# Kernel tuning notes

Measured on AMD Instinct MI355X. Metric: run time of the kernel, lower is better.

Reference implementation:

```python
import jax, jax.numpy as jnp
import numpy as np

HIDDEN = 1024
N_HEADS = 16
HEAD_DIM = HIDDEN // N_HEADS  # 64; RoPE applied only to first HEAD_DIM channels (head 0)
NUM_BUCKETS = 32
MAX_DISTANCE = 128
MLP_HIDDEN = 4 * HIDDEN
B, N = 2, 2048


def _rotate_half(x):
    # interleaved pairs [a0,b0,a1,b1,...] -> [-b0,a0,-b1,a1,...]
    sh = x.shape
    xr = x.reshape(sh[:-1] + (sh[-1] // 2, 2))
    x1, x2 = xr[..., 0], xr[..., 1]
    return jnp.stack([-x2, x1], axis=-1).reshape(sh)


def _rel_bucket(n, num_buckets=NUM_BUCKETS, max_distance=MAX_DISTANCE):
    # bidirectional T5 bucketing
    ctx = jnp.arange(n)[:, None]
    mem = jnp.arange(n)[None, :]
    rp = mem - ctx  # [n, n]
    nb = num_buckets // 2
    buckets = jnp.where(rp > 0, nb, 0)
    rp = jnp.abs(rp)
    max_exact = nb // 2
    is_small = rp < max_exact
    log_ratio = jnp.log(jnp.maximum(rp, 1).astype(jnp.float32) / max_exact)
    rpl = max_exact + (log_ratio / np.log(max_distance / max_exact) * (nb - max_exact)).astype(jnp.int32)
    rpl = jnp.minimum(rpl, nb - 1)
    return buckets + jnp.where(is_small, rp, rpl)


def _ln(x, eps=1e-6):
    # LayerNorm without affine (DiT elementwise_affine=False)
    m = jnp.mean(x, axis=-1, keepdims=True)
    v = jnp.mean(jnp.square(x - m), axis=-1, keepdims=True)
    return (x - m) * jax.lax.rsqrt(v + eps)


def setup_inputs() -> dict:
    key = jax.random.key(0)
    ks = jax.random.split(key, 12)
    s = 0.02
    return {
        "x": jax.random.normal(ks[0], (B, N, HIDDEN), dtype=jnp.float32),
        "c": jax.random.normal(ks[1], (B, HIDDEN), dtype=jnp.float32),
        "w_ada": jax.random.normal(ks[2], (HIDDEN, 6 * HIDDEN), dtype=jnp.float32) * s,
        "b_ada": jnp.zeros((6 * HIDDEN,), dtype=jnp.float32),
        "w_qkv": jax.random.normal(ks[3], (HIDDEN, 3 * HIDDEN), dtype=jnp.float32) * s,
        "b_qkv": jnp.zeros((3 * HIDDEN,), dtype=jnp.float32),
        "w_out": jax.random.normal(ks[4], (HIDDEN, HIDDEN), dtype=jnp.float32) * s,
        "b_out": jnp.zeros((HIDDEN,), dtype=jnp.float32),
        "rel_table": jax.random.normal(ks[5], (NUM_BUCKETS, N_HEADS), dtype=jnp.float32) * s,
        "w_mlp1": jax.random.normal(ks[6], (HIDDEN, MLP_HIDDEN), dtype=jnp.float32) * s,
        "b_mlp1": jnp.zeros((MLP_HIDDEN,), dtype=jnp.float32),
        "w_mlp2": jax.random.normal(ks[7], (MLP_HIDDEN, HIDDEN), dtype=jnp.float32) * s,
        "b_mlp2": jnp.zeros((HIDDEN,), dtype=jnp.float32),
    }


def reference(x, c, w_ada, b_ada, w_qkv, b_qkv, w_out, b_out, rel_table,
              w_mlp1, b_mlp1, w_mlp2, b_mlp2):
    Bb, n, hid = x.shape
    hd = HEAD_DIM

    # AdaLN-Zero modulation params from conditioning
    mod = jax.nn.silu(c) @ w_ada + b_ada  # [B, 6*hid]
    sh_msa, sc_msa, g_msa, sh_mlp, sc_mlp, g_mlp = jnp.split(mod, 6, axis=-1)

    # --- attention branch ---
    h = _ln(x) * (1.0 + sc_msa[:, None, :]) + sh_msa[:, None, :]
    qkv = h @ w_qkv + b_qkv
    q, k, v = jnp.split(qkv, 3, axis=-1)  # each [B, N, hid]

    # partial RoPE: only first head_dim channels (head 0), interleaved-duplicated freqs
    t = jnp.arange(n, dtype=jnp.float32)
    inv_freq = 1.0 / (10000.0 ** (jnp.arange(0, hd, 2, dtype=jnp.float32) / hd))
    fr = t[:, None] * inv_freq[None, :]               # [N, hd/2]
    fr = jnp.stack([fr, fr], axis=-1).reshape(n, hd)  # [N, hd] interleaved dup
    cos, sin = jnp.cos(fr)[None], jnp.sin(fr)[None]

    def partial_rope(a):
        r, u = a[..., :hd], a[..., hd:]
        r = r * cos + _rotate_half(r) * sin
        return jnp.concatenate([r, u], axis=-1)

    q = partial_rope(q)
    k = partial_rope(k)

    qh = q.reshape(Bb, n, N_HEADS, hd)
    kh = k.reshape(Bb, n, N_HEADS, hd)
    vh = v.reshape(Bb, n, N_HEADS, hd)

    scores = jnp.einsum('bqhd,bkhd->bhqk', qh, kh) / np.float32(np.sqrt(hd))
    bias = rel_table[_rel_bucket(n)]                 # [N, N, H]
    scores = scores + jnp.transpose(bias, (2, 0, 1))[None]  # [1,H,N,N]
    attn = jax.nn.softmax(scores, axis=-1)
    ctxv = jnp.einsum('bhqk,bkhd->bqhd', attn, vh).reshape(Bb, n, hid)
    attn_out = ctxv @ w_out + b_out
    x = x + g_msa[:, None, :] * attn_out

    # --- MLP branch ---
    h2 = _ln(x) * (1.0 + sc_mlp[:, None, :]) + sh_mlp[:, None, :]
    m = jax.nn.gelu(h2 @ w_mlp1 + b_mlp1, approximate=True) @ w_mlp2 + b_mlp2
    return x + g_mlp[:, None, :] * m
```

## Files before the change

### kernel.cpp

```cpp
#include <hip/hip_runtime.h>
#include <hip/hip_bf16.h>

#define SEQ 2048

typedef float f32x4 __attribute__((ext_vector_type(4)));
typedef float f32x16 __attribute__((ext_vector_type(16)));
typedef short short8 __attribute__((ext_vector_type(8)));
typedef int int4v __attribute__((ext_vector_type(4)));

static __device__ __forceinline__ unsigned short f2bf(float f) {
  __hip_bfloat16 h = __float2bfloat16(f);
  unsigned short u;
  __builtin_memcpy(&u, &h, 2);
  return u;
}
static __device__ __forceinline__ float bf2f(unsigned short u) {
  __hip_bfloat16 h;
  __builtin_memcpy(&h, &u, 2);
  return __bfloat162float(h);
}
static __device__ __forceinline__ void gload16(const void* g, void* l) {
  __builtin_amdgcn_global_load_lds(
      (const __attribute__((address_space(1))) void*)g,
      (__attribute__((address_space(3))) void*)l, 16, 0, 0);
}
static __device__ __forceinline__ float gelu_t(float x) {
  float t = x * x;
  float z = x * fmaf(0.1029442695044937f, t, 2.3021181827964594f);
  return x * __builtin_amdgcn_rcpf(1.f + exp2f(-z));
}
static __device__ __forceinline__ unsigned int cvtpk(float lo, float hi) {
  unsigned int r;
  asm("v_cvt_pk_bf16_f32 %0, %1, %2" : "=v"(r) : "v"(lo), "v"(hi));
  return r;
}
static __device__ __forceinline__ void rope_pair(short8& v, int m, int i, float pos) {
  const float fr = exp2f(-(float)(2 * i) * (13.287712379549449f / 64.f));
  const float ang = pos * fr;
  const float sn = sinf(ang), cs = cosf(ang);
  const float x0 = bf2f((unsigned short)v[2 * m]);
  const float x1 = bf2f((unsigned short)v[2 * m + 1]);
  v[2 * m] = (short)f2bf(x0 * cs - x1 * sn);
  v[2 * m + 1] = (short)f2bf(x1 * cs + x0 * sn);
}


#define SOFTMAX_M0 16.0f
__global__ void prep_transpose(const float* __restrict__ w_qkv, const float* __restrict__ w_out,
                               const float* __restrict__ w_mlp1, const float* __restrict__ w_mlp2,
                               unsigned short* __restrict__ dq, unsigned short* __restrict__ dwo,
                               unsigned short* __restrict__ dm1, unsigned short* __restrict__ dm2,
                               const float* __restrict__ c, float* __restrict__ siluc,
                               const float* __restrict__ rel_table, float* __restrict__ brp) {
  const int bid = blockIdx.x;
  const int t = threadIdx.x;
  if (bid >= 12288) {
    const int pb = bid - 12288;
    if (pb < 8) {
      int i = pb * 256 + t;
      float v = c[i];
      siluc[i] = v / (1.f + expf(-v));
    } else {
      int idx = (pb - 8) * 256 + t;
      int h = idx >> 12, pos = idx & 4095;
      int rp = pos - 2047;
      int bucket = rp > 0 ? 16 : 0;
      int a = rp < 0 ? -rp : rp;
      int bi;
      if (a < 8) {
        bi = a;
      } else {
        bi = 8 + (int)(logf((float)a / 8.f) / 2.772588722239781f * 8.f);
        if (bi > 15) bi = 15;
      }
      brp[idx] = rel_table[(bucket + bi) * 16 + h] * 1.4426950408889634f - SOFTMAX_M0;
    }
    return;
  }
  __shared__ float tile[32][33];
  const float* src;
  unsigned short* dst;
  int K, N, NT, r;
  if (bid < 3072) {
    src = w_qkv; dst = dq; K = 1024; N = 3072; NT = 96; r = bid;
  } else if (bid < 4096) {
    src = w_out; dst = dwo; K = 1024; N = 1024; NT = 32; r = bid - 3072;
  } else if (bid < 8192) {
    src = w_mlp1; dst = dm1; K = 1024; N = 4096; NT = 128; r = bid - 4096;
  } else {
    src = w_mlp2; dst = dm2; K = 4096; N = 1024; NT = 32; r = bid - 8192;
  }
  const int nt = r % NT, kt = r / NT;
  const int col = t & 31, r0 = t >> 5;
#pragma unroll
  for (int i = 0; i < 4; ++i) {
    int rr = r0 + i * 8;
    tile[rr][col] = src[(size_t)(kt * 32 + rr) * N + nt * 32 + col];
  }
  __syncthreads();
#pragma unroll
  for (int i = 0; i < 4; ++i) {
    int rr = r0 + i * 8;
    dst[(size_t)(nt * 32 + rr) * K + kt * 32 + col] = f2bf(tile[col][rr]);
  }
}

__global__ void mod_part_k(const float* __restrict__ siluc, const float* __restrict__ w_ada,
                           float* __restrict__ part) {
  int gid = blockIdx.x * 256 + threadIdx.x;
  int kc = gid / 12288;
  int idx = gid - kc * 12288;
  int b = idx / 6144;
  int j = idx - b * 6144;
  const float* cp = siluc + b * 1024 + kc * 64;
  const float* wp = w_ada + (size_t)kc * 64 * 6144 + j;
  float acc = 0.f;
#pragma unroll 8
  for (int k = 0; k < 64; ++k) acc += cp[k] * wp[(size_t)k * 6144];
  part[gid] = acc;
}

__global__ void mod_reduce_k(const float* __restrict__ part, const float* __restrict__ b_ada,
                             float* __restrict__ mod) {
  int idx = blockIdx.x * 256 + threadIdx.x;
  int j = idx % 6144;
  float a = b_ada[j];
#pragma unroll
  for (int kc = 0; kc < 16; ++kc) a += part[kc * 12288 + idx];
  mod[idx] = a;
}

__global__ void ln_mod(const float* __restrict__ x, const float* __restrict__ mod,
                       unsigned short* __restrict__ out, int sh_off, int sc_off) {
  int row = blockIdx.x;
  int b = row >> 11;
  int t = threadIdx.x;
  const float4 v = ((const float4*)(x + (size_t)row * 1024))[t];
  float s1 = v.x + v.y + v.z + v.w;
  float s2 = v.x * v.x + v.y * v.y + v.z * v.z + v.w * v.w;
#pragma unroll
  for (int off = 32; off; off >>= 1) {
    s1 += __shfl_xor(s1, off);
    s2 += __shfl_xor(s2, off);
  }
  __shared__ float red[8];
  int w = t >> 6, lane = t & 63;
  if (lane == 0) { red[w] = s1; red[4 + w] = s2; }
  __syncthreads();
  s1 = red[0] + red[1] + red[2] + red[3];
  s2 = red[4] + red[5] + red[6] + red[7];
  float mean = s1 * (1.f / 1024.f);
  float var = s2 * (1.f / 1024.f) - mean * mean;
  float rstd = rsqrtf(var + 1e-6f);
  const float* mb = mod + (size_t)b * 6144;
  int col = t * 4;
  ushort4 o4;
  o4.x = f2bf((v.x - mean) * rstd * (1.f + mb[sc_off + col + 0]) + mb[sh_off + col + 0]);
  o4.y = f2bf((v.y - mean) * rstd * (1.f + mb[sc_off + col + 1]) + mb[sh_off + col + 1]);
  o4.z = f2bf((v.z - mean) * rstd * (1.f + mb[sc_off + col + 2]) + mb[sh_off + col + 2]);
  o4.w = f2bf((v.w - mean) * rstd * (1.f + mb[sc_off + col + 3]) + mb[sh_off + col + 3]);
  *((ushort4*)(out + (size_t)row * 1024 + col)) = o4;
}

__global__ void krope_fix(unsigned short* __restrict__ kpk) {
  const int gid = blockIdx.x * 256 + threadIdx.x;
  const int i = gid & 31;
  const int l31 = (gid >> 5) & 31;
  const int kt = (gid >> 10) & 63;
  const int b = gid >> 16;
  const int d = 2 * i;
  const int bh = b * 16;
  const size_t addr = (((size_t)(bh * 64 + kt) * 4 + (d >> 4)) * 512) +
                      (((d >> 3) & 1) * 32 + l31) * 8 + (d & 7);
  unsigned int pv = *(unsigned int*)(kpk + addr);
  const float x0 = bf2f((unsigned short)(pv & 0xFFFF));
  const float x1 = bf2f((unsigned short)(pv >> 16));
  const float fr = exp2f(-(float)d * (13.287712379549449f / 64.f));
  const float ang = (float)(kt * 32 + l31) * fr;
  const float sn = sinf(ang), cs = cosf(ang);
  *(unsigned int*)(kpk + addr) =
      (unsigned int)f2bf(x0 * cs - x1 * sn) | ((unsigned int)f2bf(x1 * cs + x0 * sn) << 16);
}

template <int MODE, int BM, int BN, int PIPE>
__global__ __launch_bounds__(256) void gemm_bt(
    const unsigned short* __restrict__ A, const unsigned short* __restrict__ Bt,
    const float* __restrict__ bias, void* __restrict__ outp, const float* __restrict__ res,
    const float* __restrict__ mod, int goff, int N, int K,
    unsigned short* __restrict__ kpkp, unsigned short* __restrict__ vpkp) {
  constexpr int NBUF = PIPE ? 2 : 1;
  __shared__ __align__(16) unsigned short a_lds[NBUF][BM * 64];
  __shared__ __align__(16) unsigned short b_lds[NBUF][BN * 64];
  constexpr int WM = BM / 2, WN = BN / 2;
  constexpr int MT = WM / 16, NT = WN / 16;
  const int t = threadIdx.x;
  const int lane = t & 63;
  const int l15 = lane & 15, l4 = lane >> 4;
  const int w = t >> 6;
  const int wr = w >> 1, wc = w & 1;
  const int gx = gridDim.x;
  const int nwg = gx * gridDim.y;
  int wg = blockIdx.y * gx + blockIdx.x;
  wg = (wg & 7) * (nwg >> 3) + (wg >> 3);
  const int by = wg / gx, bx = wg - by * gx;
  const int rowA0 = by * BM;
  const int rowB0 = bx * BN;
  const int wub = t & ~63;

  f32x4 acc[MT][NT];
#pragma unroll
  for (int m = 0; m < MT; ++m)
#pragma unroll
    for (int n = 0; n < NT; ++n) acc[m][n] = (f32x4){0.f, 0.f, 0.f, 0.f};

  auto stage = [&](int buf, int kt) {
#pragma unroll
    for (int rnd = 0; rnd < BM / 32; ++rnd) {
      const int idx = rnd * 256 + t;
      const int row = idx >> 3;
      const int cb = ((idx & 7) << 4) ^ ((row & 7) << 4);
      const char* sa = (const char*)(A + (size_t)(rowA0 + row) * K + kt) + cb;
      gload16(sa, (char*)(&a_lds[buf][0]) + (size_t)(rnd * 256 + wub) * 16);
    }
#pragma unroll
    for (int rnd = 0; rnd < BN / 32; ++rnd) {
      const int idx = rnd * 256 + t;
      const int row = idx >> 3;
      const int cb = ((idx & 7) << 4) ^ ((row & 7) << 4);
      const char* sb = (const char*)(Bt + (size_t)(rowB0 + row) * K + kt) + cb;
      gload16(sb, (char*)(&b_lds[buf][0]) + (size_t)(rnd * 256 + wub) * 16);
    }
  };

  auto compute = [&](int buf) {
#pragma unroll
    for (int kb = 0; kb < 2; ++kb) {
      short8 af[MT], bfr[NT];
#pragma unroll
      for (int m = 0; m < MT; ++m) {
        int row = wr * WM + m * 16 + l15;
        int cb = (kb * 64 + l4 * 16) ^ ((row & 7) << 4);
        af[m] = *(const short8*)((const char*)(&a_lds[buf][0]) + row * 128 + cb);
      }
#pragma unroll
      for (int n = 0; n < NT; ++n) {
        int row = wc * WN + n * 16 + l15;
        int cb = (kb * 64 + l4 * 16) ^ ((row & 7) << 4);
        bfr[n] = *(const short8*)((const char*)(&b_lds[buf][0]) + row * 128 + cb);
      }
      __builtin_amdgcn_s_setprio(1);
#pragma unroll
      for (int m = 0; m < MT; ++m)
#pragma unroll
        for (int n = 0; n < NT; ++n)
          acc[m][n] = __builtin_amdgcn_mfma_f32_16x16x32_bf16(af[m], bfr[n], acc[m][n], 0, 0, 0);
      __builtin_amdgcn_s_setprio(0);
    }
  };

  if (PIPE) {
    stage(0, 0);
    __syncthreads();
    int cur = 0;
    for (int kt = 0; kt < K; kt += 64) {
      if (kt + 64 < K) stage(cur ^ 1, kt + 64);
      compute(cur);
      __syncthreads();
      cur ^= 1;
    }
  } else {
    for (int kt = 0; kt < K; kt += 64) {
      stage(0, kt);
      __syncthreads();
      compute(0);
      __syncthreads();
    }
  }

#pragma unroll
  for (int n = 0; n < NT; ++n) {
    const int col = rowB0 + wc * WN + n * 16 + l15;
    const float bv = bias[col];
#pragma unroll
    for (int m = 0; m < MT; ++m) {
      const int row0 = rowA0 + wr * WM + m * 16 + l4 * 4;
#pragma unroll
      for (int r = 0; r < 4; ++r) {
        float v = acc[m][n][r] + bv;
        if (MODE == 0) {
          ((unsigned short*)outp)[(size_t)(row0 + r) * N + col] = f2bf(v);
        } else if (MODE == 1) {
          ((unsigned short*)outp)[(size_t)(row0 + r) * N + col] = f2bf(gelu_t(v));
        } else if (MODE == 2) {
          const size_t o = (size_t)(row0 + r) * N + col;
          float g = mod[(size_t)((row0 + r) >> 11) * 6144 + goff + col];
          ((float*)outp)[o] = res[o] + g * v;
        } else {
          const int rr = row0 + r;
          if (rowB0 < 1024) {
            ((unsigned short*)outp)[(size_t)rr * N + col] = f2bf(v);
          } else if (rowB0 < 2048) {
            const int bb = rr >> 11, krow = rr & 2047;
            const int colk = col - 1024;
            const int hh = colk >> 6, d = colk & 63;
            const int bh2 = bb * 16 + hh;
            const size_t addr = (((size_t)(bh2 * 64 + (krow >> 5)) * 4 + (d >> 4)) * 512) +
                                (((d >> 3) & 1) * 32 + (krow & 31)) * 8 + (d & 7);
            kpkp[addr] = f2bf(v);
          } else {
            const int bb = rr >> 11, krow = rr & 2047;
            const int colv = col - 2048;
            const int hh = colv >> 6, d = colv & 63;
            const int bh2 = bb * 16 + hh;
            const int r5 = krow & 31;
            const int f = (d >> 5) * 2 + (r5 >> 4);
            const size_t addr = (((size_t)(bh2 * 64 + (krow >> 5)) * 4 + f) * 512) +
                                (((r5 >> 3) & 1) * 32 + (d & 31)) * 8 + (r5 & 7);
            vpkp[addr] = f2bf(v);
          }
        }
      }
    }
  }
}

__global__ __launch_bounds__(256) void attn_k(const unsigned short* __restrict__ qkv,
                                              const unsigned short* __restrict__ kpk,
                                              const unsigned short* __restrict__ vpk,
                                              const float* __restrict__ brp_all,
                                              unsigned short* __restrict__ ctxv) {
  const int t = threadIdx.x;
  const int w = t >> 6;
  const int lane = t & 63;
  const int l31 = lane & 31;
  const int hi = lane >> 5;
  const int wg = blockIdx.x;
  const int xcd = wg & 7, idx = wg >> 3;
  const int bh = xcd * 4 + (idx >> 4);
  const int qt = idx & 15;
  const int b = bh >> 4, h = bh & 15;
  const int qw = qt * 128 + w * 32;
  const float SC = 0.125f * 1.4426950408889634f;
  const float* brp = brp_all + (size_t)h * 4096;

  short8 qfr[4];
  {
    const unsigned short* qrow = qkv + (size_t)(b * SEQ + qw + l31) * 3072 + h * 64 + hi * 8;
#pragma unroll
    for (int kk = 0; kk < 4; ++kk) qfr[kk] = *(const short8*)(qrow + kk * 16);
    if (h == 0) {
      const float pos = (float)(qw + l31);
#pragma unroll
      for (int kk = 0; kk < 4; ++kk) {
        const int d0 = kk * 16 + hi * 8;
#pragma unroll
        for (int m = 0; m < 4; ++m) rope_pair(qfr[kk], m, (d0 >> 1) + m, pos);
      }
    }
  }
  const float bfar_pos = brp[4095], bfar_neg = brp[0];
  const float* bql = brp + 2047 + 4 * hi - (qw + l31);

  short8 ones;
#pragma unroll
  for (int i = 0; i < 8; ++i) ones[i] = (short)0x3F80;

  const unsigned short* kp = kpk + ((size_t)(bh * 64)) * 2048 + lane * 8;
  const unsigned short* vp = vpk + ((size_t)(bh * 64)) * 2048 + lane * 8;

  short8 kfrA[4], vfrA[4], kfrB[4], vfrB[4];
#pragma unroll
  for (int s = 0; s < 4; ++s) {
    kfrA[s] = *(const short8*)(kp + s * 512);
    vfrA[s] = *(const short8*)(vp + s * 512);
  }
  kp += 2048;
  vp += 2048;

  f32x16 oacc0 = {}, oacc1 = {}, lacc = {};
  int kbase = 0;

#define ATTN_TILE(KF, VF, KFN, VFN)                                                       \
  do {                                                                                    \
    KFN[0] = *(const short8*)(kp);                                                        \
    KFN[1] = *(const short8*)(kp + 512);                                                  \
    KFN[2] = *(const short8*)(kp + 1024);                                                 \
    KFN[3] = *(const short8*)(kp + 1536);                                                 \
    VFN[0] = *(const short8*)(vp);                                                        \
    VFN[1] = *(const short8*)(vp + 512);                                                  \
    VFN[2] = *(const short8*)(vp + 1024);                                                 \
    VFN[3] = *(const short8*)(vp + 1536);                                                 \
    kp += 2048;                                                                           \
    vp += 2048;                                                                           \
    f32x16 sacc = {};                                                                     \
    sacc = __builtin_amdgcn_mfma_f32_32x32x16_bf16(KF[0], qfr[0], sacc, 0, 0, 0);         \
    sacc = __builtin_amdgcn_mfma_f32_32x32x16_bf16(KF[1], qfr[1], sacc, 0, 0, 0);         \
    sacc = __builtin_amdgcn_mfma_f32_32x32x16_bf16(KF[2], qfr[2], sacc, 0, 0, 0);         \
    sacc = __builtin_amdgcn_mfma_f32_32x32x16_bf16(KF[3], qfr[3], sacc, 0, 0, 0);         \
    float p[16];                                                                          \
    const int dd = kbase - qw;                                                            \
    if (dd >= 128 || dd <= -128) {                                                        \
      const float bf_ = (dd > 0) ? bfar_pos : bfar_neg;                                   \
      _Pragma("unroll") for (int r = 0; r < 16; ++r)                                      \
          p[r] = __builtin_amdgcn_exp2f(fmaf(sacc[r], SC, bf_));                          \
    } else {                                                                              \
      const float* bp = bql + kbase;                                                      \
      _Pragma("unroll") for (int r = 0; r < 16; ++r)                                      \
          p[r] = __builtin_amdgcn_exp2f(fmaf(sacc[r], SC, bp[(r & 3) + 8 * (r >> 2)]));   \
    }                                                                                     \
    unsigned int x0 = cvtpk(p[0], p[1]), x1 = cvtpk(p[2], p[3]);                          \
    unsigned int y0 = cvtpk(p[4], p[5]), y1 = cvtpk(p[6], p[7]);                          \
    asm("v_permlane32_swap_b32 %0, %1" : "+v"(x0), "+v"(y0));                             \
    asm("v_permlane32_swap_b32 %0, %1" : "+v"(x1), "+v"(y1));                             \
    unsigned int x2 = cvtpk(p[8], p[9]), x3 = cvtpk(p[10], p[11]);                        \
    unsigned int y2 = cvtpk(p[12], p[13]), y3 = cvtpk(p[14], p[15]);                      \
    asm("v_permlane32_swap_b32 %0, %1" : "+v"(x2), "+v"(y2));                             \
    asm("v_permlane32_swap_b32 %0, %1" : "+v"(x3), "+v"(y3));                             \
    int4v pi0 = {(int)x0, (int)x1, (int)y0, (int)y1};                                     \
    int4v pi1 = {(int)x2, (int)x3, (int)y2, (int)y3};                                     \
    short8 pf0 = __builtin_bit_cast(short8, pi0);                                         \
    short8 pf1 = __builtin_bit_cast(short8, pi1);                                         \
    lacc = __builtin_amdgcn_mfma_f32_32x32x16_bf16(ones, pf0, lacc, 0, 0, 0);             \
    lacc = __builtin_amdgcn_mfma_f32_32x32x16_bf16(ones, pf1, lacc, 0, 0, 0);             \
    oacc0 = __builtin_amdgcn_mfma_f32_32x32x16_bf16(VF[0], pf0, oacc0, 0, 0, 0);          \
    oacc0 = __builtin_amdgcn_mfma_f32_32x32x16_bf16(VF[1], pf1, oacc0, 0, 0, 0);          \
    oacc1 = __builtin_amdgcn_mfma_f32_32x32x16_bf16(VF[2], pf0, oacc1, 0, 0, 0);          \
    oacc1 = __builtin_amdgcn_mfma_f32_32x32x16_bf16(VF[3], pf1, oacc1, 0, 0, 0);          \
    kbase += 32;                                                                          \
  } while (0)

#pragma unroll 1
  for (int it = 0; it < 32; ++it) {
    ATTN_TILE(kfrA, vfrA, kfrB, vfrB);
    ATTN_TILE(kfrB, vfrB, kfrA, vfrA);
  }
#undef ATTN_TILE

  const float inv = 1.f / lacc[0];
  unsigned short* orow = ctxv + (size_t)(b * SEQ + qw + l31) * 1024 + h * 64;
#pragma unroll
  for (int r = 0; r < 16; r += 2) {
    const int d = (r & 3) + 8 * (r >> 2) + 4 * hi;
    *(unsigned int*)(orow + d) = cvtpk(oacc0[r] * inv, oacc0[r + 1] * inv);
    *(unsigned int*)(orow + 32 + d) = cvtpk(oacc1[r] * inv, oacc1[r + 1] * inv);
  }
}

extern "C" void kernel_launch(void* const* d_in, const int* in_sizes, int n_in, void* d_out,
                              int out_size, void* d_ws, size_t ws_size, hipStream_t stream) {
  (void)in_sizes; (void)n_in; (void)out_size; (void)ws_size;
  const float* x = (const float*)d_in[0];
  const float* c = (const float*)d_in[1];
  const float* w_ada = (const float*)d_in[2];
  const float* b_ada = (const float*)d_in[3];
  const float* w_qkv = (const float*)d_in[4];
  const float* b_qkv = (const float*)d_in[5];
  const float* w_out = (const float*)d_in[6];
  const float* b_out = (const float*)d_in[7];
  const float* rel_t = (const float*)d_in[8];
  const float* w_mlp1 = (const float*)d_in[9];
  const float* b_mlp1 = (const float*)d_in[10];
  const float* w_mlp2 = (const float*)d_in[11];
  const float* b_mlp2 = (const float*)d_in[12];
  float* out = (float*)d_out;
  char* ws = (char*)d_ws;

  constexpr size_t OFF_WQKVT = 0;
  constexpr size_t OFF_WOUTT = OFF_WQKVT + (size_t)3072 * 1024 * 2;
  constexpr size_t OFF_WM1T = OFF_WOUTT + (size_t)1024 * 1024 * 2;
  constexpr size_t OFF_WM2T = OFF_WM1T + (size_t)4096 * 1024 * 2;
  constexpr size_t OFF_H = OFF_WM2T + (size_t)1024 * 4096 * 2;
  constexpr size_t OFF_QKV = OFF_H + (size_t)4096 * 1024 * 2;
  constexpr size_t OFF_VT = OFF_QKV + (size_t)4096 * 3072 * 2;
  constexpr size_t OFF_CTXV = OFF_VT + (size_t)32 * 64 * 2048 * 2;
  constexpr size_t OFF_MID = OFF_CTXV + (size_t)4096 * 1024 * 2;
  constexpr size_t OFF_SILU = OFF_MID + (size_t)4096 * 4096 * 2;
  constexpr size_t OFF_MOD = OFF_SILU + 2048 * 4;
  constexpr size_t OFF_BRP = OFF_MOD + 12288 * 4;
  constexpr size_t OFF_PART = OFF_BRP + 65536 * 4;

  unsigned short* wqkvT = (unsigned short*)(ws + OFF_WQKVT);
  unsigned short* woutT = (unsigned short*)(ws + OFF_WOUTT);
  unsigned short* wm1T = (unsigned short*)(ws + OFF_WM1T);
  unsigned short* wm2T = (unsigned short*)(ws + OFF_WM2T);
  unsigned short* hbuf = (unsigned short*)(ws + OFF_H);
  unsigned short* qkvbuf = (unsigned short*)(ws + OFF_QKV);
  unsigned short* vpkbuf = (unsigned short*)(ws + OFF_VT);
  unsigned short* ctxvbuf = (unsigned short*)(ws + OFF_CTXV);
  unsigned short* midbuf = (unsigned short*)(ws + OFF_MID);
  unsigned short* kpkbuf = (unsigned short*)(ws + OFF_MID);
  float* siluc = (float*)(ws + OFF_SILU);
  float* modb = (float*)(ws + OFF_MOD);
  float* brp = (float*)(ws + OFF_BRP);
  float* part = (float*)(ws + OFF_PART);

  prep_transpose<<<12552, 256, 0, stream>>>(w_qkv, w_out, w_mlp1, w_mlp2, wqkvT, woutT, wm1T,
                                            wm2T, c, siluc, rel_t, brp);
  mod_part_k<<<768, 256, 0, stream>>>(siluc, w_ada, part);
  mod_reduce_k<<<48, 256, 0, stream>>>(part, b_ada, modb);

  ln_mod<<<4096, 256, 0, stream>>>(x, modb, hbuf, 0, 1024);
  gemm_bt<3, 128, 128, 0><<<dim3(24, 32), 256, 0, stream>>>(hbuf, wqkvT, b_qkv, qkvbuf, nullptr,
                                                            nullptr, 0, 3072, 1024, kpkbuf,
                                                            vpkbuf);
  krope_fix<<<512, 256, 0, stream>>>(kpkbuf);
  attn_k<<<512, 256, 0, stream>>>(qkvbuf, kpkbuf, vpkbuf, brp, ctxvbuf);
  gemm_bt<2, 64, 64, 1><<<dim3(16, 64), 256, 0, stream>>>(ctxvbuf, woutT, b_out, out, x, modb,
                                                          2048, 1024, 1024, nullptr, nullptr);
  ln_mod<<<4096, 256, 0, stream>>>(out, modb, hbuf, 3072, 4096);
  gemm_bt<1, 128, 128, 0><<<dim3(32, 32), 256, 0, stream>>>(hbuf, wm1T, b_mlp1, midbuf, nullptr,
                                                            nullptr, 0, 4096, 1024, nullptr,
                                                            nullptr);
  gemm_bt<2, 64, 64, 1><<<dim3(16, 64), 256, 0, stream>>>(midbuf, wm2T, b_mlp2, out, out, modb,
                                                          5120, 1024, 4096, nullptr, nullptr);
}
```

Baseline: 238.7 us.

## Software-pipeline attention loop: overlap next-tile QK MFMA with current softmax and PV

Restructures the attention inner loop so the QK^T MFMA for tile i+1 is issued before the exp/convert/permlane softmax and PV MFMAs of tile i. This lets the matrix core run while the vector ALU computes exponentials, hiding MFMA latency. K and V loads are split and issued later, just after their registers are consumed, and a prologue/epilogue handles the first and last tiles. It adds another 16-register score accumulator, which raises VGPR pressure and may lower occupancy.

```diff
diff --git a/kernel.cpp b/kernel.cpp
--- a/kernel.cpp
+++ b/kernel.cpp
@@ -376,65 +376,100 @@
   }
   kp += 2048;
   vp += 2048;
-
-  f32x16 oacc0 = {}, oacc1 = {}, lacc = {};
-  int kbase = 0;
-
-#define ATTN_TILE(KF, VF, KFN, VFN)                                                       \
-  do {                                                                                    \
-    KFN[0] = *(const short8*)(kp);                                                        \
-    KFN[1] = *(const short8*)(kp + 512);                                                  \
-    KFN[2] = *(const short8*)(kp + 1024);                                                 \
-    KFN[3] = *(const short8*)(kp + 1536);                                                 \
-    VFN[0] = *(const short8*)(vp);                                                        \
-    VFN[1] = *(const short8*)(vp + 512);                                                  \
-    VFN[2] = *(const short8*)(vp + 1024);                                                 \
-    VFN[3] = *(const short8*)(vp + 1536);                                                 \
-    kp += 2048;                                                                           \
-    vp += 2048;                                                                           \
-    f32x16 sacc = {};                                                                     \
-    sacc = __builtin_amdgcn_mfma_f32_32x32x16_bf16(KF[0], qfr[0], sacc, 0, 0, 0);         \
-    sacc = __builtin_amdgcn_mfma_f32_32x32x16_bf16(KF[1], qfr[1], sacc, 0, 0, 0);         \
-    sacc = __builtin_amdgcn_mfma_f32_32x32x16_bf16(KF[2], qfr[2], sacc, 0, 0, 0);         \
-    sacc = __builtin_amdgcn_mfma_f32_32x32x16_bf16(KF[3], qfr[3], sacc, 0, 0, 0);         \
-    float p[16];                                                                          \
-    const int dd = kbase - qw;                                                            \
-    if (dd >= 128 || dd <= -128) {                                                        \
-      const float bf_ = (dd > 0) ? bfar_pos : bfar_neg;                                   \
-      _Pragma("unroll") for (int r = 0; r < 16; ++r)                                      \
-          p[r] = __builtin_amdgcn_exp2f(fmaf(sacc[r], SC, bf_));                          \
-    } else {                                                                              \
-      const float* bp = bql + kbase;                                                      \
-      _Pragma("unroll") for (int r = 0; r < 16; ++r)                                      \
-          p[r] = __builtin_amdgcn_exp2f(fmaf(sacc[r], SC, bp[(r & 3) + 8 * (r >> 2)]));   \
-    }                                                                                     \
-    unsigned int x0 = cvtpk(p[0], p[1]), x1 = cvtpk(p[2], p[3]);                          \
-    unsigned int y0 = cvtpk(p[4], p[5]), y1 = cvtpk(p[6], p[7]);                          \
-    asm("v_permlane32_swap_b32 %0, %1" : "+v"(x0), "+v"(y0));                             \
-    asm("v_permlane32_swap_b32 %0, %1" : "+v"(x1), "+v"(y1));                             \
-    unsigned int x2 = cvtpk(p[8], p[9]), x3 = cvtpk(p[10], p[11]);                        \
-    unsigned int y2 = cvtpk(p[12], p[13]), y3 = cvtpk(p[14], p[15]);                      \
-    asm("v_permlane32_swap_b32 %0, %1" : "+v"(x2), "+v"(y2));                             \
-    asm("v_permlane32_swap_b32 %0, %1" : "+v"(x3), "+v"(y3));                             \
-    int4v pi0 = {(int)x0, (int)x1, (int)y0, (int)y1};                                     \
-    int4v pi1 = {(int)x2, (int)x3, (int)y2, (int)y3};                                     \
-    short8 pf0 = __builtin_bit_cast(short8, pi0);                                         \
-    short8 pf1 = __builtin_bit_cast(short8, pi1);                                         \
-    lacc = __builtin_amdgcn_mfma_f32_32x32x16_bf16(ones, pf0, lacc, 0, 0, 0);             \
-    lacc = __builtin_amdgcn_mfma_f32_32x32x16_bf16(ones, pf1, lacc, 0, 0, 0);             \
-    oacc0 = __builtin_amdgcn_mfma_f32_32x32x16_bf16(VF[0], pf0, oacc0, 0, 0, 0);          \
-    oacc0 = __builtin_amdgcn_mfma_f32_32x32x16_bf16(VF[1], pf1, oacc0, 0, 0, 0);          \
-    oacc1 = __builtin_amdgcn_mfma_f32_32x32x16_bf16(VF[2], pf0, oacc1, 0, 0, 0);          \
-    oacc1 = __builtin_amdgcn_mfma_f32_32x32x16_bf16(VF[3], pf1, oacc1, 0, 0, 0);          \
-    kbase += 32;                                                                          \
+#pragma unroll
+  for (int s = 0; s < 4; ++s) {
+    kfrB[s] = *(const short8*)(kp + s * 512);
+    vfrB[s] = *(const short8*)(vp + s * 512);
+  }
+  kp += 2048;
+  vp += 2048;
+
+  f32x16 oacc0 = {}, oacc1 = {}, lacc = {}, saccA = {}, saccB = {};
+
+#define QK_COMP(SACC, KF)                                                           \
+  do {                                                                              \
+    f32x16 z_ = {};                                                                 \
+    z_ = __builtin_amdgcn_mfma_f32_32x32x16_bf16(KF[0], qfr[0], z_, 0, 0, 0);       \
+    z_ = __builtin_amdgcn_mfma_f32_32x32x16_bf16(KF[1], qfr[1], z_, 0, 0, 0);       \
+    z_ = __builtin_amdgcn_mfma_f32_32x32x16_bf16(KF[2], qfr[2], z_, 0, 0, 0);       \
+    z_ = __builtin_amdgcn_mfma_f32_32x32x16_bf16(KF[3], qfr[3], z_, 0, 0, 0);       \
+    SACC = z_;                                                                      \
   } while (0)
 
+#define LOADK(KF)                                                                   \
+  do {                                                                              \
+    KF[0] = *(const short8*)(kp);                                                   \
+    KF[1] = *(const short8*)(kp + 512);                                             \
+    KF[2] = *(const short8*)(kp + 1024);                                            \
+    KF[3] = *(const short8*)(kp + 1536);                                            \
+  } while (0)
+
+#define LOADV(VF)                                                                   \
+  do {                                                                              \
+    VF[0] = *(const short8*)(vp);                                                   \
+    VF[1] = *(const short8*)(vp + 512);                                             \
+    VF[2] = *(const short8*)(vp + 1024);                                            \
+    VF[3] = *(const short8*)(vp + 1536);                                            \
+  } while (0)
+
+#define SM_PV(SACC, VF, KB)                                                              \
+  do {                                                                                   \
+    float p[16];                                                                         \
+    const int dd = (KB)-qw;                                                              \
+    if (dd >= 128 || dd <= -128) {                                                       \
+      const float bf_ = (dd > 0) ? bfar_pos : bfar_neg;                                  \
+      _Pragma("unroll") for (int r = 0; r < 16; ++r)                                     \
+          p[r] = __builtin_amdgcn_exp2f(fmaf(SACC[r], SC, bf_));                         \
+    } else {                                                                             \
+      const float* bp = bql + (KB);                                                      \
+      _Pragma("unroll") for (int r = 0; r < 16; ++r)                                     \
+          p[r] = __builtin_amdgcn_exp2f(fmaf(SACC[r], SC, bp[(r & 3) + 8 * (r >> 2)]));  \
+    }                                                                                    \
+    unsigned int x0 = cvtpk(p[0], p[1]), x1 = cvtpk(p[2], p[3]);                         \
+    unsigned int y0 = cvtpk(p[4], p[5]), y1 = cvtpk(p[6], p[7]);                         \
+    asm("v_permlane32_swap_b32 %0, %1" : "+v"(x0), "+v"(y0));                            \
+    asm("v_permlane32_swap_b32 %0, %1" : "+v"(x1), "+v"(y1));                            \
+    unsigned int x2 = cvtpk(p[8], p[9]), x3 = cvtpk(p[10], p[11]);                       \
+    unsigned int y2 = cvtpk(p[12], p[13]), y3 = cvtpk(p[14], p[15]);                     \
+    asm("v_permlane32_swap_b32 %0, %1" : "+v"(x2), "+v"(y2));                            \
+    asm("v_permlane32_swap_b32 %0, %1" : "+v"(x3), "+v"(y3));                            \
+    int4v pi0 = {(int)x0, (int)x1, (int)y0, (int)y1};                                    \
+    int4v pi1 = {(int)x2, (int)x3, (int)y2, (int)y3};                                    \
+    short8 pf0 = __builtin_bit_cast(short8, pi0);                                        \
+    short8 pf1 = __builtin_bit_cast(short8, pi1);                                        \
+    lacc = __builtin_amdgcn_mfma_f32_32x32x16_bf16(ones, pf0, lacc, 0, 0, 0);            \
+    lacc = __builtin_amdgcn_mfma_f32_32x32x16_bf16(ones, pf1, lacc, 0, 0, 0);            \
+    oacc0 = __builtin_amdgcn_mfma_f32_32x32x16_bf16(VF[0], pf0, oacc0, 0, 0, 0);         \
+    oacc0 = __builtin_amdgcn_mfma_f32_32x32x16_bf16(VF[1], pf1, oacc0, 0, 0, 0);         \
+    oacc1 = __builtin_amdgcn_mfma_f32_32x32x16_bf16(VF[2], pf0, oacc1, 0, 0, 0);         \
+    oacc1 = __builtin_amdgcn_mfma_f32_32x32x16_bf16(VF[3], pf1, oacc1, 0, 0, 0);         \
+  } while (0)
+
+  QK_COMP(saccA, kfrA);
+
 #pragma unroll 1
-  for (int it = 0; it < 32; ++it) {
-    ATTN_TILE(kfrA, vfrA, kfrB, vfrB);
-    ATTN_TILE(kfrB, vfrB, kfrA, vfrA);
-  }
-#undef ATTN_TILE
+  for (int it = 0; it < 31; ++it) {
+    QK_COMP(saccB, kfrB);
+    LOADK(kfrA);
+    SM_PV(saccA, vfrA, it * 64);
+    LOADV(vfrA);
+    kp += 2048;
+    vp += 2048;
+    QK_COMP(saccA, kfrA);
+    LOADK(kfrB);
+    SM_PV(saccB, vfrB, it * 64 + 32);
+    LOADV(vfrB);
+    kp += 2048;
+    vp += 2048;
+  }
+  QK_COMP(saccB, kfrB);
+  SM_PV(saccA, vfrA, 1984);
+  SM_PV(saccB, vfrB, 2016);
+
+#undef QK_COMP
+#undef LOADK
+#undef LOADV
+#undef SM_PV
 
   const float inv = 1.f / lacc[0];
   unsigned short* orow = ctxv + (size_t)(b * SEQ + qw + l31) * 1024 + h * 64;
```

Result: no change. 235.6 us (-1.3%).
